# Performance work log

Hardware: AMD Instinct MI355X
Metric: run time of the kernel (lower is better)

## Reference

```python
import jax, jax.numpy as jnp
import numpy as np
import math

B, L, D = 32, 1024, 64
MASK_VALUE = -1000000.0

def setup_inputs() -> dict:
    key = jax.random.key(0)
    kq, kk, kv, kl = jax.random.split(key, 4)
    queries = jax.random.normal(kq, (B, L, D), dtype=jnp.float32)
    keys = jax.random.normal(kk, (B, L, D), dtype=jnp.float32)
    values = jax.random.normal(kv, (B, L, D), dtype=jnp.float32)
    valid_lens = jax.random.randint(kl, (B,), 1, L + 1, dtype=jnp.int32)
    return {"queries": queries, "keys": keys, "values": values, "valid_lens": valid_lens}

def reference(queries, keys, values, valid_lens):
    d = queries.shape[-1]
    # scores: [B, Lq, Lk]
    scores = jnp.einsum("bqd,bkd->bqk", queries, keys) / math.sqrt(d)
    # per-batch valid length mask over the key axis (last axis)
    kv_len = keys.shape[1]
    mask = jnp.arange(kv_len)[None, None, :] < valid_lens[:, None, None]
    masked = jnp.where(mask, scores, MASK_VALUE)
    attn_w = jax.nn.softmax(masked, axis=-1)
    # dropout prob is 0.0 (eval-equivalent), so apply weights directly
    attn_score = jnp.einsum("bqk,bkd->bqd", attn_w, values)
    return (attn_score, attn_w)
```

## Files before the change

### kernel.cpp

```cpp
#include <hip/hip_runtime.h>

#define BB 32
#define LL 1024
#define DD 64

typedef short bf16x8 __attribute__((ext_vector_type(8)));
typedef float f32x4 __attribute__((ext_vector_type(4)));

static __device__ __forceinline__ ushort f2bf(float x) {
  union { float f; unsigned u; } c; c.f = x;
  unsigned r = c.u + 0x7FFF + ((c.u >> 16) & 1);
  return (ushort)(r >> 16);
}

static __device__ __forceinline__ bf16x8 pack8(float4 a, float4 b) {
  union { ushort u[8]; bf16x8 v; } r;
  r.u[0] = f2bf(a.x); r.u[1] = f2bf(a.y); r.u[2] = f2bf(a.z); r.u[3] = f2bf(a.w);
  r.u[4] = f2bf(b.x); r.u[5] = f2bf(b.y); r.u[6] = f2bf(b.z); r.u[7] = f2bf(b.w);
  return r.v;
}

__global__ __launch_bounds__(256) void prep(const float* __restrict__ K,
                                            const float* __restrict__ V,
                                            ushort* __restrict__ Kbf,
                                            ushort* __restrict__ VT) {
  const int b = blockIdx.x, kt = blockIdx.y, t = threadIdx.x;

  const float* Ks = K + ((size_t)b * LL + kt * 64) * DD;
  ushort* Kd = Kbf + ((size_t)b * LL + kt * 64) * DD;
#pragma unroll
  for (int i = 0; i < 4; ++i) {
    int e = (i * 256 + t) * 4;
    float4 v = *(const float4*)(Ks + e);
    union { ushort u[4]; uint2 q; } p;
    p.u[0] = f2bf(v.x); p.u[1] = f2bf(v.y); p.u[2] = f2bf(v.z); p.u[3] = f2bf(v.w);
    *(uint2*)(Kd + e) = p.q;
  }

  __shared__ ushort T[64][72];
  const float* Vb = V + ((size_t)b * LL + kt * 64) * DD;
#pragma unroll
  for (int i = 0; i < 4; ++i) {
    int kr = (t >> 4) + i * 16;
    int d0 = (t & 15) * 4;
    float4 v = *(const float4*)(Vb + kr * DD + d0);
    T[d0 + 0][kr] = f2bf(v.x);
    T[d0 + 1][kr] = f2bf(v.y);
    T[d0 + 2][kr] = f2bf(v.z);
    T[d0 + 3][kr] = f2bf(v.w);
  }
  __syncthreads();
  ushort* VTb = VT + (size_t)b * DD * LL + kt * 64;
#pragma unroll
  for (int i = 0; i < 2; ++i) {
    int d = (t >> 3) + i * 32;
    int s8 = (t & 7) * 8;
    *(uint4*)(VTb + (size_t)d * LL + s8) = *(const uint4*)(&T[d][s8]);
  }
}

#define WSTR 1028
__global__ __launch_bounds__(256, 4) void attn(
    const float* __restrict__ Q, const ushort* __restrict__ Kbf,
    const int* __restrict__ vlen, const ushort* __restrict__ VTg,
    float* __restrict__ outS, float* __restrict__ outW) {
  __shared__ __align__(16) ushort Ws[16][WSTR];
  __shared__ float redm[4][16];
  __shared__ float reds[4][16];

  const int b = blockIdx.x >> 6;
  const int q0 = (blockIdx.x & 63) << 4;
  const int tid = threadIdx.x;
  const int wv = tid >> 6, lane = tid & 63;
  const int quad = lane >> 4, n16 = lane & 15;
  const int vl = vlen[b];

  const float* Qp = Q + (size_t)(b * LL + q0 + n16) * DD + quad * 8;
  bf16x8 a0 = pack8(*(const float4*)Qp, *(const float4*)(Qp + 4));
  bf16x8 a1 = pack8(*(const float4*)(Qp + 32), *(const float4*)(Qp + 36));

  const ushort* Kb = Kbf + (size_t)b * LL * DD;
  const int kb = wv * 256 + n16;

  f32x4 acc[16];
#pragma unroll
  for (int t = 0; t < 16; ++t) {
    const ushort* Kp = Kb + (size_t)(kb + t * 16) * DD + quad * 8;
    f32x4 c = {0.f, 0.f, 0.f, 0.f};
    c = __builtin_amdgcn_mfma_f32_16x16x32_bf16(a0, *(const bf16x8*)Kp, c, 0, 0, 0);
    c = __builtin_amdgcn_mfma_f32_16x16x32_bf16(a1, *(const bf16x8*)(Kp + 32), c, 0, 0, 0);
    acc[t] = c;
  }

  float pm[4] = {-3.0e38f, -3.0e38f, -3.0e38f, -3.0e38f};
#pragma unroll
  for (int t = 0; t < 16; ++t) {
    const bool valid = (kb + t * 16) < vl;
#pragma unroll
    for (int r = 0; r < 4; ++r) {
      float v = valid ? acc[t][r] * 0.125f : -1.0e6f;
      acc[t][r] = v;
      pm[r] = fmaxf(pm[r], v);
    }
  }
#pragma unroll
  for (int off = 1; off < 16; off <<= 1) {
#pragma unroll
    for (int r = 0; r < 4; ++r) pm[r] = fmaxf(pm[r], __shfl_xor(pm[r], off));
  }
  if (n16 == 0) {
#pragma unroll
    for (int r = 0; r < 4; ++r) redm[wv][quad * 4 + r] = pm[r];
  }
  __syncthreads();
  float gm[4];
#pragma unroll
  for (int r = 0; r < 4; ++r) {
    int row = quad * 4 + r;
    gm[r] = fmaxf(fmaxf(redm[0][row], redm[1][row]),
                  fmaxf(redm[2][row], redm[3][row]));
  }
  float ps[4] = {0.f, 0.f, 0.f, 0.f};
#pragma unroll
  for (int t = 0; t < 16; ++t) {
#pragma unroll
    for (int r = 0; r < 4; ++r) {
      float e = __expf(acc[t][r] - gm[r]);
      acc[t][r] = e;
      ps[r] += e;
    }
  }
#pragma unroll
  for (int off = 1; off < 16; off <<= 1) {
#pragma unroll
    for (int r = 0; r < 4; ++r) ps[r] += __shfl_xor(ps[r], off);
  }
  if (n16 == 0) {
#pragma unroll
    for (int r = 0; r < 4; ++r) reds[wv][quad * 4 + r] = ps[r];
  }
  __syncthreads();
  float inv[4];
#pragma unroll
  for (int r = 0; r < 4; ++r) {
    int row = quad * 4 + r;
    inv[r] = 1.0f / (reds[0][row] + reds[1][row] + reds[2][row] + reds[3][row]);
  }

#pragma unroll
  for (int t = 0; t < 16; ++t) {
#pragma unroll
    for (int r = 0; r < 4; ++r)
      Ws[quad * 4 + r][kb + t * 16] = f2bf(acc[t][r] * inv[r]);
  }
  __syncthreads();

  f32x4 o = {0.f, 0.f, 0.f, 0.f};
  const ushort* VTb = VTg + (size_t)b * DD * LL + (size_t)(wv * 16 + n16) * LL;
#pragma unroll
  for (int g = 0; g < 4; ++g) {
    bf16x8 af[8], bv[8];
#pragma unroll
    for (int i = 0; i < 8; ++i) {
      int k0 = (g * 8 + i) * 32 + quad * 8;
      bv[i] = *(const bf16x8*)(VTb + k0);
      af[i] = *(const bf16x8*)(&Ws[n16][k0]);
    }
#pragma unroll
    for (int i = 0; i < 8; ++i)
      o = __builtin_amdgcn_mfma_f32_16x16x32_bf16(af[i], bv[i], o, 0, 0, 0);
  }
#pragma unroll
  for (int r = 0; r < 4; ++r) {
    outS[(size_t)(b * LL + q0 + quad * 4 + r) * DD + wv * 16 + n16] = o[r];
  }

  {
    float* dstW = outW + (size_t)b * LL * LL + (size_t)q0 * LL;
#pragma unroll
    for (int i = 0; i < 16; ++i) {
      int j = i * 256 + tid;
      int row = j >> 8, c4 = j & 255;
      uint2 u = *(const uint2*)(&Ws[row][c4 * 4]);
      union { unsigned q[4]; float4 v; } ov;
      ov.q[0] = u.x << 16; ov.q[1] = u.x & 0xffff0000u;
      ov.q[2] = u.y << 16; ov.q[3] = u.y & 0xffff0000u;
      *(float4*)(dstW + (size_t)row * LL + c4 * 4) = ov.v;
    }
  }
}

extern "C" void kernel_launch(void* const* d_in, const int* in_sizes, int n_in,
                              void* d_out, int out_size, void* d_ws, size_t ws_size,
                              hipStream_t stream) {
  const float* Q = (const float*)d_in[0];
  const float* K = (const float*)d_in[1];
  const float* V = (const float*)d_in[2];
  const int* vl = (const int*)d_in[3];
  float* outS = (float*)d_out;
  float* outW = outS + (size_t)BB * LL * DD;
  ushort* VT = (ushort*)d_ws;
  ushort* Kbf = VT + (size_t)BB * DD * LL;

  prep<<<dim3(BB, 16), 256, 0, stream>>>(K, V, Kbf, VT);
  attn<<<dim3(BB * 64), 256, 0, stream>>>(Q, Kbf, vl, VT, outS, outW);
}
```

Baseline: 212.8 us.

## Merge softmax reductions into one barrier, prefetch V, nontemporal weight stores

Each wave now computes its local max and local exp-sum before a single barrier, then rescales the partial sums with the wave maxima. This removes one of the two block-wide barriers in the softmax. V-transpose fragments are prefetched from global memory before the softmax and then double-buffered across the PV loop, which uses two independent MFMA accumulators to break the dependency chain. Attention-weight outputs are written with nontemporal stores, and Q/K conversion uses the packed bf16 intrinsics. The cost is more registers held live, which may reduce occupancy.

```diff
diff --git a/kernel.cpp b/kernel.cpp
--- a/kernel.cpp
+++ b/kernel.cpp
@@ -1,4 +1,5 @@
 #include <hip/hip_runtime.h>
+#include <hip/hip_bf16.h>
 
 #define BB 32
 #define LL 1024
@@ -14,9 +15,11 @@
 }
 
 static __device__ __forceinline__ bf16x8 pack8(float4 a, float4 b) {
-  union { ushort u[8]; bf16x8 v; } r;
-  r.u[0] = f2bf(a.x); r.u[1] = f2bf(a.y); r.u[2] = f2bf(a.z); r.u[3] = f2bf(a.w);
-  r.u[4] = f2bf(b.x); r.u[5] = f2bf(b.y); r.u[6] = f2bf(b.z); r.u[7] = f2bf(b.w);
+  union { __hip_bfloat162 h[4]; bf16x8 v; } r;
+  r.h[0] = __float22bfloat162_rn({a.x, a.y});
+  r.h[1] = __float22bfloat162_rn({a.z, a.w});
+  r.h[2] = __float22bfloat162_rn({b.x, b.y});
+  r.h[3] = __float22bfloat162_rn({b.z, b.w});
   return r.v;
 }
 
@@ -32,8 +35,9 @@
   for (int i = 0; i < 4; ++i) {
     int e = (i * 256 + t) * 4;
     float4 v = *(const float4*)(Ks + e);
-    union { ushort u[4]; uint2 q; } p;
-    p.u[0] = f2bf(v.x); p.u[1] = f2bf(v.y); p.u[2] = f2bf(v.z); p.u[3] = f2bf(v.w);
+    union { __hip_bfloat162 h[2]; uint2 q; } p;
+    p.h[0] = __float22bfloat162_rn({v.x, v.y});
+    p.h[1] = __float22bfloat162_rn({v.z, v.w});
     *(uint2*)(Kd + e) = p.q;
   }
 
@@ -92,6 +96,11 @@
     acc[t] = c;
   }
 
+  const ushort* VTb = VTg + (size_t)b * DD * LL + (size_t)(wv * 16 + n16) * LL;
+  bf16x8 bvp[8];
+#pragma unroll
+  for (int i = 0; i < 8; ++i) bvp[i] = *(const bf16x8*)(VTb + i * 32 + quad * 8);
+
   float pm[4] = {-3.0e38f, -3.0e38f, -3.0e38f, -3.0e38f};
 #pragma unroll
   for (int t = 0; t < 16; ++t) {
@@ -108,71 +117,75 @@
 #pragma unroll
     for (int r = 0; r < 4; ++r) pm[r] = fmaxf(pm[r], __shfl_xor(pm[r], off));
   }
+  float ps[4] = {0.f, 0.f, 0.f, 0.f};
+#pragma unroll
+  for (int t = 0; t < 16; ++t) {
+#pragma unroll
+    for (int r = 0; r < 4; ++r) {
+      float e = __expf(acc[t][r] - pm[r]);
+      acc[t][r] = e;
+      ps[r] += e;
+    }
+  }
+#pragma unroll
+  for (int off = 1; off < 16; off <<= 1) {
+#pragma unroll
+    for (int r = 0; r < 4; ++r) ps[r] += __shfl_xor(ps[r], off);
+  }
   if (n16 == 0) {
 #pragma unroll
-    for (int r = 0; r < 4; ++r) redm[wv][quad * 4 + r] = pm[r];
+    for (int r = 0; r < 4; ++r) {
+      redm[wv][quad * 4 + r] = pm[r];
+      reds[wv][quad * 4 + r] = ps[r];
+    }
   }
   __syncthreads();
-  float gm[4];
+
+  float f[4];
 #pragma unroll
   for (int r = 0; r < 4; ++r) {
     int row = quad * 4 + r;
-    gm[r] = fmaxf(fmaxf(redm[0][row], redm[1][row]),
-                  fmaxf(redm[2][row], redm[3][row]));
-  }
-  float ps[4] = {0.f, 0.f, 0.f, 0.f};
-#pragma unroll
-  for (int t = 0; t < 16; ++t) {
-#pragma unroll
-    for (int r = 0; r < 4; ++r) {
-      float e = __expf(acc[t][r] - gm[r]);
-      acc[t][r] = e;
-      ps[r] += e;
-    }
-  }
-#pragma unroll
-  for (int off = 1; off < 16; off <<= 1) {
-#pragma unroll
-    for (int r = 0; r < 4; ++r) ps[r] += __shfl_xor(ps[r], off);
-  }
-  if (n16 == 0) {
-#pragma unroll
-    for (int r = 0; r < 4; ++r) reds[wv][quad * 4 + r] = ps[r];
+    float m0 = redm[0][row], m1 = redm[1][row], m2 = redm[2][row], m3 = redm[3][row];
+    float gm = fmaxf(fmaxf(m0, m1), fmaxf(m2, m3));
+    float tot = reds[0][row] * __expf(m0 - gm) + reds[1][row] * __expf(m1 - gm) +
+                reds[2][row] * __expf(m2 - gm) + reds[3][row] * __expf(m3 - gm);
+    f[r] = __expf(pm[r] - gm) / tot;
+  }
+
+#pragma unroll
+  for (int t = 0; t < 16; ++t) {
+#pragma unroll
+    for (int r = 0; r < 4; ++r)
+      Ws[quad * 4 + r][kb + t * 16] = f2bf(acc[t][r] * f[r]);
   }
   __syncthreads();
-  float inv[4];
+
+  f32x4 o0 = {0.f, 0.f, 0.f, 0.f}, o1 = {0.f, 0.f, 0.f, 0.f};
+#pragma unroll
+  for (int g = 0; g < 4; ++g) {
+    bf16x8 bvn[8];
+    if (g < 3) {
+#pragma unroll
+      for (int i = 0; i < 8; ++i)
+        bvn[i] = *(const bf16x8*)(VTb + ((g + 1) * 8 + i) * 32 + quad * 8);
+    }
+    bf16x8 af[8];
+#pragma unroll
+    for (int i = 0; i < 8; ++i)
+      af[i] = *(const bf16x8*)(&Ws[n16][(g * 8 + i) * 32 + quad * 8]);
+#pragma unroll
+    for (int i = 0; i < 8; ++i) {
+      if (i & 1)
+        o1 = __builtin_amdgcn_mfma_f32_16x16x32_bf16(af[i], bvp[i], o1, 0, 0, 0);
+      else
+        o0 = __builtin_amdgcn_mfma_f32_16x16x32_bf16(af[i], bvp[i], o0, 0, 0, 0);
+    }
+#pragma unroll
+    for (int i = 0; i < 8; ++i) bvp[i] = bvn[i];
+  }
 #pragma unroll
   for (int r = 0; r < 4; ++r) {
-    int row = quad * 4 + r;
-    inv[r] = 1.0f / (reds[0][row] + reds[1][row] + reds[2][row] + reds[3][row]);
-  }
-
-#pragma unroll
-  for (int t = 0; t < 16; ++t) {
-#pragma unroll
-    for (int r = 0; r < 4; ++r)
-      Ws[quad * 4 + r][kb + t * 16] = f2bf(acc[t][r] * inv[r]);
-  }
-  __syncthreads();
-
-  f32x4 o = {0.f, 0.f, 0.f, 0.f};
-  const ushort* VTb = VTg + (size_t)b * DD * LL + (size_t)(wv * 16 + n16) * LL;
-#pragma unroll
-  for (int g = 0; g < 4; ++g) {
-    bf16x8 af[8], bv[8];
-#pragma unroll
-    for (int i = 0; i < 8; ++i) {
-      int k0 = (g * 8 + i) * 32 + quad * 8;
-      bv[i] = *(const bf16x8*)(VTb + k0);
-      af[i] = *(const bf16x8*)(&Ws[n16][k0]);
-    }
-#pragma unroll
-    for (int i = 0; i < 8; ++i)
-      o = __builtin_amdgcn_mfma_f32_16x16x32_bf16(af[i], bv[i], o, 0, 0, 0);
-  }
-#pragma unroll
-  for (int r = 0; r < 4; ++r) {
-    outS[(size_t)(b * LL + q0 + quad * 4 + r) * DD + wv * 16 + n16] = o[r];
+    outS[(size_t)(b * LL + q0 + quad * 4 + r) * DD + wv * 16 + n16] = o0[r] + o1[r];
   }
 
   {
@@ -182,10 +195,12 @@
       int j = i * 256 + tid;
       int row = j >> 8, c4 = j & 255;
       uint2 u = *(const uint2*)(&Ws[row][c4 * 4]);
-      union { unsigned q[4]; float4 v; } ov;
-      ov.q[0] = u.x << 16; ov.q[1] = u.x & 0xffff0000u;
-      ov.q[2] = u.y << 16; ov.q[3] = u.y & 0xffff0000u;
-      *(float4*)(dstW + (size_t)row * LL + c4 * 4) = ov.v;
+      f32x4 ov;
+      union { unsigned q; float f; } w0, w1, w2, w3;
+      w0.q = u.x << 16; w1.q = u.x & 0xffff0000u;
+      w2.q = u.y << 16; w3.q = u.y & 0xffff0000u;
+      ov[0] = w0.f; ov[1] = w1.f; ov[2] = w2.f; ov[3] = w3.f;
+      __builtin_nontemporal_store(ov, (f32x4*)(dstW + (size_t)row * LL + c4 * 4));
     }
   }
 }
```

New measurement: 226.9 us. 6.6% more time.
